# Kernel optimization log

Hardware: AMD Instinct MI355X
Metric: run time of the kernel (lower is better)

## Reference

```python
import jax, jax.numpy as jnp
import numpy as np

N, K = 4096, 256          # rays, samples per ray
V = 100000                # voxel table size
D = 64                    # field MLP hidden dim
SCALER = 7.0              # free-energy scaler from the source


def setup_inputs() -> dict:
    key = jax.random.key(0)
    ks = jax.random.split(key, 12)
    ray_start = jax.random.normal(ks[0], (N, 3), jnp.float32)
    rd = jax.random.normal(ks[1], (N, 3), jnp.float32)
    ray_dir = rd / jnp.linalg.norm(rd, axis=-1, keepdims=True)
    sampled_depth = jnp.sort(
        0.5 + 4.0 * jax.random.uniform(ks[2], (N, K), jnp.float32), axis=-1)
    sampled_dists = 0.02 * jax.random.uniform(ks[3], (N, K), jnp.float32)
    raw = jax.random.randint(ks[4], (N, K), 0, V + V // 4)
    sampled_idx = jnp.where(raw < V, raw, -1).astype(jnp.int64)
    voxel_color = 0.1 * jax.random.normal(ks[5], (V, 3), jnp.float32)
    W1 = jax.random.normal(ks[6], (6, D), jnp.float32) * (1.0 / np.sqrt(6.0))
    b1 = jnp.zeros((D,), jnp.float32)
    w_sigma = jax.random.normal(ks[7], (D, 1), jnp.float32) * (1.0 / np.sqrt(D))
    b_sigma = jnp.zeros((1,), jnp.float32)
    W_tex = jax.random.normal(ks[8], (D, 3), jnp.float32) * (1.0 / np.sqrt(D))
    b_tex = jnp.zeros((3,), jnp.float32)
    return dict(ray_start=ray_start, ray_dir=ray_dir,
                sampled_depth=sampled_depth, sampled_dists=sampled_dists,
                sampled_idx=sampled_idx, voxel_color=voxel_color,
                W1=W1, b1=b1, w_sigma=w_sigma, b_sigma=b_sigma,
                W_tex=W_tex, b_tex=b_tex)


def reference(ray_start, ray_dir, sampled_depth, sampled_dists, sampled_idx,
              voxel_color, W1, b1, w_sigma, b_sigma, W_tex, b_tex):
    mask = sampled_idx != -1                                   # [N,K] sample_mask
    # sampled_xyz = ray(start, dir, depth); sampled_dir broadcast of ray_dir
    xyz = ray_start[:, None, :] + ray_dir[:, None, :] * sampled_depth[..., None]
    dirs = jnp.broadcast_to(ray_dir[:, None, :], xyz.shape)    # [N,K,3]
    feat = jnp.concatenate([xyz, dirs], axis=-1)               # [N,K,6]
    # field_fn: small MLP -> sigma, texture
    h = jax.nn.relu(jnp.einsum('nkf,fd->nkd', feat, W1) + b1)  # [N,K,D]
    sigma = (jnp.einsum('nkd,do->nko', h, w_sigma) + b_sigma)[..., 0]  # [N,K]
    # voxel color embedding lookup (F.embedding); res=True adds it to texture
    idx_safe = jnp.where(mask, sampled_idx, 0)
    vcol = voxel_color[idx_safe]                               # [N,K,3] gather
    texture = jnp.einsum('nkd,dc->nkc', h, W_tex) + b_tex + vcol
    # free energy; masked_scatter == zero-out where mask is False
    free_energy = jnp.where(mask,
                            jax.nn.relu(sigma) * sampled_dists * SCALER, 0.0)
    texture = jnp.where(mask[..., None], texture, 0.0)
    # alpha compositing: a = 1-exp(-fe), b = exp(-cumsum(shifted fe))
    shifted = jnp.concatenate(
        [jnp.zeros((free_energy.shape[0], 1), free_energy.dtype),
         free_energy[:, :-1]], axis=-1)
    a = 1.0 - jnp.exp(-free_energy)
    b = jnp.exp(-jnp.cumsum(shifted, axis=-1))
    probs = a * b                                              # [N,K]
    depths = jnp.sum(sampled_depth * probs, axis=-1)           # [N]
    missed = 1.0 - jnp.sum(probs, axis=-1)                     # [N]
    colors = jnp.sum(texture * probs[..., None], axis=-2)      # [N,3]
    return colors, depths, missed, probs
```

## Files before the change

kernel.cpp:

```cpp
#include <hip/hip_runtime.h>

#define K_SAMP 256
#define D_HID 64
#define SCALER_FE 7.0f

typedef _Float16 half8  __attribute__((ext_vector_type(8)));
typedef __fp16   fp16x2 __attribute__((ext_vector_type(2)));
typedef float    f32x4  __attribute__((ext_vector_type(4)));

union H8U { half8 h; uint u[4]; };
union H8P { fp16x2 h2[4]; half8 h8; };

__device__ __forceinline__ half8 h8zero() {
    half8 a;
    #pragma unroll
    for (int j = 0; j < 8; ++j) a[j] = (_Float16)0.f;
    return a;
}

#define DPP_ADD(x, ctrl, rowmask)                                              \
    (x) += __int_as_float(__builtin_amdgcn_update_dpp(                         \
        0, __float_as_int(x), (ctrl), (rowmask), 0xf, false))

__device__ __forceinline__ float dpp_scan_incl(float x) {
    DPP_ADD(x, 0x111, 0xf);
    DPP_ADD(x, 0x112, 0xf);
    DPP_ADD(x, 0x114, 0xf);
    DPP_ADD(x, 0x118, 0xf);
    DPP_ADD(x, 0x142, 0xa);
    DPP_ADD(x, 0x143, 0xc);
    return x;
}

__global__ __launch_bounds__(256, 4)
void volrend_kernel(const float* __restrict__ ray_start,
                    const float* __restrict__ ray_dir,
                    const float* __restrict__ depth,
                    const float* __restrict__ dists,
                    const int*   __restrict__ vidx,
                    const float* __restrict__ vcol_tab,
                    const float* __restrict__ W1,
                    const float* __restrict__ b1,
                    const float* __restrict__ w_sigma,
                    const float* __restrict__ b_sigma,
                    const float* __restrict__ W_tex,
                    const float* __restrict__ b_tex,
                    float* __restrict__ out_colors,
                    float* __restrict__ out_depths,
                    float* __restrict__ out_missed,
                    float* __restrict__ out_probs) {
    __shared__ uint  sFragP[4][6 * 64];
    __shared__ float sOutP[4][4 * K_SAMP];

    const int tid  = threadIdx.x;
    const int lane = tid & 63;
    const int wv   = tid >> 6;
    const int ray  = __builtin_amdgcn_readfirstlane(blockIdx.x * 4 + wv);
    const int m    = lane & 15;
    const int g    = lane >> 4;

    if (tid < 64) {
        #pragma unroll
        for (int tt = 0; tt < 4; ++tt) {
            const int dim = 8 * (m >> 2) + (m & 3) + 4 * (tt & 1) + 32 * (tt >> 1);
            half8 a = h8zero();
            if (g == 0) {
                #pragma unroll
                for (int j = 0; j < 6; ++j) a[j] = (_Float16)W1[j * D_HID + dim];
                a[6] = (_Float16)b1[dim];
            }
            H8U c; c.h = a;
            #pragma unroll
            for (int k = 0; k < 4; ++k) sFragP[k][tt * 64 + lane] = c.u[k];
        }
        half8 a2a = h8zero(), a2b = h8zero();
        if (m < 4) {
            const int c = (m >= 1) ? (m - 1) : 0;
            #pragma unroll
            for (int j = 0; j < 8; ++j) {
                const int d = 8 * g + j;
                a2a[j] = (_Float16)((m == 0) ? w_sigma[d]      : W_tex[d * 3 + c]);
                a2b[j] = (_Float16)((m == 0) ? w_sigma[d + 32] : W_tex[(d + 32) * 3 + c]);
            }
        }
        H8U ca; ca.h = a2a;
        H8U cb; cb.h = a2b;
        #pragma unroll
        for (int k = 0; k < 4; ++k) {
            sFragP[k][4 * 64 + lane] = ca.u[k];
            sFragP[k][5 * 64 + lane] = cb.u[k];
        }
    }

    const float rs0 = ray_start[ray * 3 + 0];
    const float rs1 = ray_start[ray * 3 + 1];
    const float rs2 = ray_start[ray * 3 + 2];
    const float rd0 = ray_dir[ray * 3 + 0];
    const float rd1 = ray_dir[ray * 3 + 1];
    const float rd2 = ray_dir[ray * 3 + 2];
    const float bs  = b_sigma[0];
    const float bt0 = b_tex[0], bt1 = b_tex[1], bt2 = b_tex[2];

    const size_t rayBase = (size_t)ray * K_SAMP;
    float dep_[4], dst_[4];
    int   vi_[4];
    #pragma unroll
    for (int s = 0; s < 4; ++s) {
        const int n = lane + 64 * s;
        dep_[s] = depth[rayBase + n];
        dst_[s] = dists[rayBase + n];
        vi_[s]  = vidx[rayBase + n];
    }
    bool  msk[4];
    float vc[4][3];
    #pragma unroll
    for (int s = 0; s < 4; ++s) {
        msk[s] = (vi_[s] != -1);
        const int b = (msk[s] ? vi_[s] : 0) * 3;
        vc[s][0] = vcol_tab[b + 0];
        vc[s][1] = vcol_tab[b + 1];
        vc[s][2] = vcol_tab[b + 2];
    }

    __syncthreads();

    half8 a1[4];
    #pragma unroll
    for (int tt = 0; tt < 4; ++tt) {
        H8U c;
        #pragma unroll
        for (int k = 0; k < 4; ++k) c.u[k] = sFragP[k][tt * 64 + lane];
        a1[tt] = c.h;
    }
    H8U ca, cb;
    #pragma unroll
    for (int k = 0; k < 4; ++k) {
        ca.u[k] = sFragP[k][4 * 64 + lane];
        cb.u[k] = sFragP[k][5 * 64 + lane];
    }
    const half8 a2a = ca.h;
    const half8 a2b = cb.h;

    f32x4 oinit = {0.f, 0.f, 0.f, 0.f};
    if (g == 0) { oinit[0] = bs; oinit[1] = bt0; oinit[2] = bt1; oinit[3] = bt2; }
    const f32x4 zero4 = {0.f, 0.f, 0.f, 0.f};

    const fp16x2 hc12 = __builtin_amdgcn_cvt_pkrtz(rd1, rd2);
    const fp16x2 hc3  = __builtin_amdgcn_cvt_pkrtz(1.0f, 0.0f);

    #pragma unroll 4
    for (int t = 0; t < 16; ++t) {
        const float dpt = depth[rayBase + 16 * t + m];
        const float fx = fmaf(rd0, dpt, rs0);
        const float fy = fmaf(rd1, dpt, rs1);
        const float fz = fmaf(rd2, dpt, rs2);
        H8P bb;
        bb.h2[0] = __builtin_amdgcn_cvt_pkrtz(fx, fy);
        bb.h2[1] = __builtin_amdgcn_cvt_pkrtz(fz, rd0);
        bb.h2[2] = hc12;
        bb.h2[3] = hc3;
        const f32x4 h0 = __builtin_amdgcn_mfma_f32_16x16x32_f16(a1[0], bb.h8, zero4, 0, 0, 0);
        const f32x4 h1 = __builtin_amdgcn_mfma_f32_16x16x32_f16(a1[1], bb.h8, zero4, 0, 0, 0);
        const f32x4 h2 = __builtin_amdgcn_mfma_f32_16x16x32_f16(a1[2], bb.h8, zero4, 0, 0, 0);
        const f32x4 h3 = __builtin_amdgcn_mfma_f32_16x16x32_f16(a1[3], bb.h8, zero4, 0, 0, 0);

        H8P p2a, p2b;
        p2a.h2[0] = __builtin_amdgcn_cvt_pkrtz(fmaxf(h0[0], 0.f), fmaxf(h0[1], 0.f));
        p2a.h2[1] = __builtin_amdgcn_cvt_pkrtz(fmaxf(h0[2], 0.f), fmaxf(h0[3], 0.f));
        p2a.h2[2] = __builtin_amdgcn_cvt_pkrtz(fmaxf(h1[0], 0.f), fmaxf(h1[1], 0.f));
        p2a.h2[3] = __builtin_amdgcn_cvt_pkrtz(fmaxf(h1[2], 0.f), fmaxf(h1[3], 0.f));
        p2b.h2[0] = __builtin_amdgcn_cvt_pkrtz(fmaxf(h2[0], 0.f), fmaxf(h2[1], 0.f));
        p2b.h2[1] = __builtin_amdgcn_cvt_pkrtz(fmaxf(h2[2], 0.f), fmaxf(h2[3], 0.f));
        p2b.h2[2] = __builtin_amdgcn_cvt_pkrtz(fmaxf(h3[0], 0.f), fmaxf(h3[1], 0.f));
        p2b.h2[3] = __builtin_amdgcn_cvt_pkrtz(fmaxf(h3[2], 0.f), fmaxf(h3[3], 0.f));

        f32x4 o = oinit;
        o = __builtin_amdgcn_mfma_f32_16x16x32_f16(a2a, p2a.h8, o, 0, 0, 0);
        o = __builtin_amdgcn_mfma_f32_16x16x32_f16(a2b, p2b.h8, o, 0, 0, 0);

        if (g == 0) {
            const int idx = (wv << 8) + 16 * t + m;
            sOutP[0][idx] = o[0];
            sOutP[1][idx] = o[1];
            sOutP[2][idx] = o[2];
            sOutP[3][idx] = o[3];
        }
    }

    float fe_[4], tA[4], tB[4], tC[4];
    #pragma unroll
    for (int s = 0; s < 4; ++s) {
        const int idx = (wv << 8) + lane + 64 * s;
        const float sg = sOutP[0][idx];
        const float u0 = sOutP[1][idx];
        const float u1 = sOutP[2][idx];
        const float u2 = sOutP[3][idx];
        if (msk[s]) {
            fe_[s] = fmaxf(sg, 0.f) * dst_[s] * SCALER_FE;
            tA[s] = u0 + vc[s][0];
            tB[s] = u1 + vc[s][1];
            tC[s] = u2 + vc[s][2];
        } else {
            fe_[s] = 0.f; tA[s] = 0.f; tB[s] = 0.f; tC[s] = 0.f;
        }
    }

    float incl[4], tot[4];
    #pragma unroll
    for (int s = 0; s < 4; ++s) incl[s] = dpp_scan_incl(fe_[s]);
    #pragma unroll
    for (int s = 0; s < 4; ++s) tot[s] = __shfl(incl[s], 63, 64);

    float p_[4];
    float base = 0.f;
    #pragma unroll
    for (int s = 0; s < 4; ++s) {
        const float e = base + incl[s] - fe_[s];
        p_[s] = (1.0f - __expf(-fe_[s])) * __expf(-e);
        base += tot[s];
    }
    #pragma unroll
    for (int s = 0; s < 4; ++s) {
        out_probs[rayBase + lane + 64 * s] = p_[s];
    }

    float sp = dpp_scan_incl(p_[0] + p_[1] + p_[2] + p_[3]);
    float sd = dpp_scan_incl(dep_[0] * p_[0] + dep_[1] * p_[1] +
                             dep_[2] * p_[2] + dep_[3] * p_[3]);
    float c0 = dpp_scan_incl(tA[0] * p_[0] + tA[1] * p_[1] + tA[2] * p_[2] + tA[3] * p_[3]);
    float c1 = dpp_scan_incl(tB[0] * p_[0] + tB[1] * p_[1] + tB[2] * p_[2] + tB[3] * p_[3]);
    float c2 = dpp_scan_incl(tC[0] * p_[0] + tC[1] * p_[1] + tC[2] * p_[2] + tC[3] * p_[3]);
    if (lane == 63) {
        out_colors[ray * 3 + 0] = c0;
        out_colors[ray * 3 + 1] = c1;
        out_colors[ray * 3 + 2] = c2;
        out_depths[ray] = sd;
        out_missed[ray] = 1.0f - sp;
    }
}

extern "C" void kernel_launch(void* const* d_in, const int* in_sizes, int n_in,
                              void* d_out, int out_size, void* d_ws, size_t ws_size,
                              hipStream_t stream) {
    const float* ray_start  = (const float*)d_in[0];
    const float* ray_dir    = (const float*)d_in[1];
    const float* depth      = (const float*)d_in[2];
    const float* dists      = (const float*)d_in[3];
    const int*   vidx       = (const int*)d_in[4];
    const float* vcol       = (const float*)d_in[5];
    const float* W1         = (const float*)d_in[6];
    const float* b1         = (const float*)d_in[7];
    const float* w_sigma    = (const float*)d_in[8];
    const float* b_sigma    = (const float*)d_in[9];
    const float* W_tex      = (const float*)d_in[10];
    const float* b_tex      = (const float*)d_in[11];

    const int N = in_sizes[0] / 3;
    float* out        = (float*)d_out;
    float* out_colors = out;
    float* out_depths = out + (size_t)N * 3;
    float* out_missed = out + (size_t)N * 3 + N;
    float* out_probs  = out + (size_t)N * 3 + 2 * (size_t)N;

    volrend_kernel<<<N / 4, 256, 0, stream>>>(
        ray_start, ray_dir, depth, dists, vidx, vcol,
        W1, b1, w_sigma, b_sigma, W_tex, b_tex,
        out_colors, out_depths, out_missed, out_probs);
}
```

Baseline: 19.88 us.

## Split fused kernel into per-ray MLP kernel and compositing kernel via workspace

The single fused kernel is split in two. The first is an MLP kernel that launches one block per ray, with four waves each handling 64 samples, and writes per-sample free energy and texture as float4 to a global workspace. The second is a compositing kernel that reads the workspace back and performs the scan and reductions. This aims to raise parallelism and occupancy in the MLP phase, which was serialised over 16 tiles per wave. In exchange it adds a 16 MB workspace round-trip through memory and a second kernel launch.

```diff
diff --git a/kernel.cpp b/kernel.cpp
--- a/kernel.cpp
+++ b/kernel.cpp
@@ -32,30 +32,26 @@
     return x;
 }
 
-__global__ __launch_bounds__(256, 4)
-void volrend_kernel(const float* __restrict__ ray_start,
-                    const float* __restrict__ ray_dir,
-                    const float* __restrict__ depth,
-                    const float* __restrict__ dists,
-                    const int*   __restrict__ vidx,
-                    const float* __restrict__ vcol_tab,
-                    const float* __restrict__ W1,
-                    const float* __restrict__ b1,
-                    const float* __restrict__ w_sigma,
-                    const float* __restrict__ b_sigma,
-                    const float* __restrict__ W_tex,
-                    const float* __restrict__ b_tex,
-                    float* __restrict__ out_colors,
-                    float* __restrict__ out_depths,
-                    float* __restrict__ out_missed,
-                    float* __restrict__ out_probs) {
-    __shared__ uint  sFragP[4][6 * 64];
-    __shared__ float sOutP[4][4 * K_SAMP];
+__global__ __launch_bounds__(256, 6)
+void volrend_mlp(const float* __restrict__ ray_start,
+                 const float* __restrict__ ray_dir,
+                 const float* __restrict__ depth,
+                 const float* __restrict__ dists,
+                 const int*   __restrict__ vidx,
+                 const float* __restrict__ vcol_tab,
+                 const float* __restrict__ W1,
+                 const float* __restrict__ b1,
+                 const float* __restrict__ w_sigma,
+                 const float* __restrict__ b_sigma,
+                 const float* __restrict__ W_tex,
+                 const float* __restrict__ b_tex,
+                 float4* __restrict__ ws) {
+    __shared__ uint sFragP[4][6 * 64];
 
     const int tid  = threadIdx.x;
     const int lane = tid & 63;
     const int wv   = tid >> 6;
-    const int ray  = __builtin_amdgcn_readfirstlane(blockIdx.x * 4 + wv);
+    const int ray  = blockIdx.x;
     const int m    = lane & 15;
     const int g    = lane >> 4;
 
@@ -101,27 +97,6 @@
     const float bs  = b_sigma[0];
     const float bt0 = b_tex[0], bt1 = b_tex[1], bt2 = b_tex[2];
 
-    const size_t rayBase = (size_t)ray * K_SAMP;
-    float dep_[4], dst_[4];
-    int   vi_[4];
-    #pragma unroll
-    for (int s = 0; s < 4; ++s) {
-        const int n = lane + 64 * s;
-        dep_[s] = depth[rayBase + n];
-        dst_[s] = dists[rayBase + n];
-        vi_[s]  = vidx[rayBase + n];
-    }
-    bool  msk[4];
-    float vc[4][3];
-    #pragma unroll
-    for (int s = 0; s < 4; ++s) {
-        msk[s] = (vi_[s] != -1);
-        const int b = (msk[s] ? vi_[s] : 0) * 3;
-        vc[s][0] = vcol_tab[b + 0];
-        vc[s][1] = vcol_tab[b + 1];
-        vc[s][2] = vcol_tab[b + 2];
-    }
-
     __syncthreads();
 
     half8 a1[4];
@@ -148,9 +123,12 @@
     const fp16x2 hc12 = __builtin_amdgcn_cvt_pkrtz(rd1, rd2);
     const fp16x2 hc3  = __builtin_amdgcn_cvt_pkrtz(1.0f, 0.0f);
 
-    #pragma unroll 4
-    for (int t = 0; t < 16; ++t) {
-        const float dpt = depth[rayBase + 16 * t + m];
+    const size_t rayBase = (size_t)ray * K_SAMP;
+
+    #pragma unroll
+    for (int t = 0; t < 4; ++t) {
+        const int   n   = (wv << 6) + 16 * t + m;
+        const float dpt = depth[rayBase + n];
         const float fx = fmaf(rd0, dpt, rs0);
         const float fy = fmaf(rd1, dpt, rs1);
         const float fz = fmaf(rd2, dpt, rs2);
@@ -179,30 +157,41 @@
         o = __builtin_amdgcn_mfma_f32_16x16x32_f16(a2b, p2b.h8, o, 0, 0, 0);
 
         if (g == 0) {
-            const int idx = (wv << 8) + 16 * t + m;
-            sOutP[0][idx] = o[0];
-            sOutP[1][idx] = o[1];
-            sOutP[2][idx] = o[2];
-            sOutP[3][idx] = o[3];
-        }
-    }
-
-    float fe_[4], tA[4], tB[4], tC[4];
+            const float dstv = dists[rayBase + n];
+            const int   viv  = vidx[rayBase + n];
+            const bool  mk   = (viv != -1);
+            const int   vb   = (mk ? viv : 0) * 3;
+            float fe = 0.f, tA = 0.f, tB = 0.f, tC = 0.f;
+            if (mk) {
+                fe = fmaxf(o[0], 0.f) * dstv * SCALER_FE;
+                tA = o[1] + vcol_tab[vb + 0];
+                tB = o[2] + vcol_tab[vb + 1];
+                tC = o[3] + vcol_tab[vb + 2];
+            }
+            ws[rayBase + n] = make_float4(fe, tA, tB, tC);
+        }
+    }
+}
+
+__global__ __launch_bounds__(256, 8)
+void volrend_comp(const float4* __restrict__ ws,
+                  const float*  __restrict__ depth,
+                  float* __restrict__ out_colors,
+                  float* __restrict__ out_depths,
+                  float* __restrict__ out_missed,
+                  float* __restrict__ out_probs) {
+    const int lane = threadIdx.x & 63;
+    const int wv   = threadIdx.x >> 6;
+    const int ray  = __builtin_amdgcn_readfirstlane(blockIdx.x * 4 + wv);
+    const size_t rayBase = (size_t)ray * K_SAMP;
+
+    float fe_[4], tA[4], tB[4], tC[4], dep_[4];
     #pragma unroll
     for (int s = 0; s < 4; ++s) {
-        const int idx = (wv << 8) + lane + 64 * s;
-        const float sg = sOutP[0][idx];
-        const float u0 = sOutP[1][idx];
-        const float u1 = sOutP[2][idx];
-        const float u2 = sOutP[3][idx];
-        if (msk[s]) {
-            fe_[s] = fmaxf(sg, 0.f) * dst_[s] * SCALER_FE;
-            tA[s] = u0 + vc[s][0];
-            tB[s] = u1 + vc[s][1];
-            tC[s] = u2 + vc[s][2];
-        } else {
-            fe_[s] = 0.f; tA[s] = 0.f; tB[s] = 0.f; tC[s] = 0.f;
-        }
+        const int n = lane + 64 * s;
+        const float4 f4 = ws[rayBase + n];
+        dep_[s] = depth[rayBase + n];
+        fe_[s] = f4.x; tA[s] = f4.y; tB[s] = f4.z; tC[s] = f4.w;
     }
 
     float incl[4], tot[4];
@@ -261,9 +250,11 @@
     float* out_depths = out + (size_t)N * 3;
     float* out_missed = out + (size_t)N * 3 + N;
     float* out_probs  = out + (size_t)N * 3 + 2 * (size_t)N;
-
-    volrend_kernel<<<N / 4, 256, 0, stream>>>(
+    float4* ws = (float4*)d_ws;
+
+    volrend_mlp<<<N, 256, 0, stream>>>(
         ray_start, ray_dir, depth, dists, vidx, vcol,
-        W1, b1, w_sigma, b_sigma, W_tex, b_tex,
-        out_colors, out_depths, out_missed, out_probs);
-}
+        W1, b1, w_sigma, b_sigma, W_tex, b_tex, ws);
+    volrend_comp<<<N / 4, 256, 0, stream>>>(
+        ws, depth, out_colors, out_depths, out_missed, out_probs);
+}
```

Result: slower. 29.03 us (+46.0%).

## Switch MLP matmuls from 16x16x32 to 32x32x16 MFMA tiles

Applied to the files above, without the earlier changes.

Replaces the 16x16x32 f16 MFMA layout with 32x32x16 MFMAs that process 32 samples per step. The first layer now takes 2 MFMAs per 32 samples instead of 4 per 16, and the second layer takes 4 chained MFMAs per 32 samples instead of 2 per 16. Weight fragments are rebuilt for the new operand layout, and the upper half-wave gets zero B inputs because K only covers 8 features. The instruction count per sample drops slightly, but the larger MFMAs have longer latency, need 16-wide accumulators that raise register pressure, and waste half the K dimension on zeros.

```diff
diff --git a/kernel.cpp b/kernel.cpp
--- a/kernel.cpp
+++ b/kernel.cpp
@@ -6,7 +6,7 @@
 
 typedef _Float16 half8  __attribute__((ext_vector_type(8)));
 typedef __fp16   fp16x2 __attribute__((ext_vector_type(2)));
-typedef float    f32x4  __attribute__((ext_vector_type(4)));
+typedef float    f32x16 __attribute__((ext_vector_type(16)));
 
 union H8U { half8 h; uint u[4]; };
 union H8P { fp16x2 h2[4]; half8 h8; };
@@ -56,39 +56,38 @@
     const int lane = tid & 63;
     const int wv   = tid >> 6;
     const int ray  = __builtin_amdgcn_readfirstlane(blockIdx.x * 4 + wv);
-    const int m    = lane & 15;
-    const int g    = lane >> 4;
+    const int col  = lane & 31;
+    const int g2   = lane >> 5;
 
     if (tid < 64) {
-        #pragma unroll
-        for (int tt = 0; tt < 4; ++tt) {
-            const int dim = 8 * (m >> 2) + (m & 3) + 4 * (tt & 1) + 32 * (tt >> 1);
+        const int x = lane & 31;
+        #pragma unroll
+        for (int T = 0; T < 2; ++T) {
             half8 a = h8zero();
-            if (g == 0) {
+            if (lane < 32) {
+                const int dim = 16 * (x >> 3) + 8 * ((x >> 2) & 1) + 4 * T + (x & 3);
                 #pragma unroll
                 for (int j = 0; j < 6; ++j) a[j] = (_Float16)W1[j * D_HID + dim];
                 a[6] = (_Float16)b1[dim];
             }
             H8U c; c.h = a;
             #pragma unroll
-            for (int k = 0; k < 4; ++k) sFragP[k][tt * 64 + lane] = c.u[k];
-        }
-        half8 a2a = h8zero(), a2b = h8zero();
-        if (m < 4) {
-            const int c = (m >= 1) ? (m - 1) : 0;
+            for (int k = 0; k < 4; ++k) sFragP[k][T * 64 + lane] = c.u[k];
+        }
+        #pragma unroll
+        for (int q = 0; q < 4; ++q) {
+            half8 a = h8zero();
+            if (x < 4) {
+                const int dbase = 16 * q + 8 * (lane >> 5);
+                #pragma unroll
+                for (int j = 0; j < 8; ++j) {
+                    const int d = dbase + j;
+                    a[j] = (_Float16)((x == 0) ? w_sigma[d] : W_tex[d * 3 + (x - 1)]);
+                }
+            }
+            H8U c; c.h = a;
             #pragma unroll
-            for (int j = 0; j < 8; ++j) {
-                const int d = 8 * g + j;
-                a2a[j] = (_Float16)((m == 0) ? w_sigma[d]      : W_tex[d * 3 + c]);
-                a2b[j] = (_Float16)((m == 0) ? w_sigma[d + 32] : W_tex[(d + 32) * 3 + c]);
-            }
-        }
-        H8U ca; ca.h = a2a;
-        H8U cb; cb.h = a2b;
-        #pragma unroll
-        for (int k = 0; k < 4; ++k) {
-            sFragP[k][4 * 64 + lane] = ca.u[k];
-            sFragP[k][5 * 64 + lane] = cb.u[k];
+            for (int k = 0; k < 4; ++k) sFragP[k][(2 + q) * 64 + lane] = c.u[k];
         }
     }
 
@@ -124,62 +123,66 @@
 
     __syncthreads();
 
-    half8 a1[4];
-    #pragma unroll
-    for (int tt = 0; tt < 4; ++tt) {
+    half8 a1[2], a2[4];
+    #pragma unroll
+    for (int T = 0; T < 2; ++T) {
         H8U c;
         #pragma unroll
-        for (int k = 0; k < 4; ++k) c.u[k] = sFragP[k][tt * 64 + lane];
-        a1[tt] = c.h;
-    }
-    H8U ca, cb;
-    #pragma unroll
-    for (int k = 0; k < 4; ++k) {
-        ca.u[k] = sFragP[k][4 * 64 + lane];
-        cb.u[k] = sFragP[k][5 * 64 + lane];
-    }
-    const half8 a2a = ca.h;
-    const half8 a2b = cb.h;
-
-    f32x4 oinit = {0.f, 0.f, 0.f, 0.f};
-    if (g == 0) { oinit[0] = bs; oinit[1] = bt0; oinit[2] = bt1; oinit[3] = bt2; }
-    const f32x4 zero4 = {0.f, 0.f, 0.f, 0.f};
+        for (int k = 0; k < 4; ++k) c.u[k] = sFragP[k][T * 64 + lane];
+        a1[T] = c.h;
+    }
+    #pragma unroll
+    for (int q = 0; q < 4; ++q) {
+        H8U c;
+        #pragma unroll
+        for (int k = 0; k < 4; ++k) c.u[k] = sFragP[k][(2 + q) * 64 + lane];
+        a2[q] = c.h;
+    }
+
+    f32x16 zero16;
+    #pragma unroll
+    for (int k = 0; k < 16; ++k) zero16[k] = 0.f;
+    f32x16 oinit = zero16;
+    if (lane < 32) { oinit[0] = bs; oinit[1] = bt0; oinit[2] = bt1; oinit[3] = bt2; }
 
     const fp16x2 hc12 = __builtin_amdgcn_cvt_pkrtz(rd1, rd2);
     const fp16x2 hc3  = __builtin_amdgcn_cvt_pkrtz(1.0f, 0.0f);
-
-    #pragma unroll 4
-    for (int t = 0; t < 16; ++t) {
-        const float dpt = depth[rayBase + 16 * t + m];
+    const half8  bnull = h8zero();
+
+    #pragma unroll 2
+    for (int t = 0; t < 8; ++t) {
+        const int   n   = 32 * t + col;
+        const float dpt = depth[rayBase + n];
         const float fx = fmaf(rd0, dpt, rs0);
         const float fy = fmaf(rd1, dpt, rs1);
         const float fz = fmaf(rd2, dpt, rs2);
-        H8P bb;
-        bb.h2[0] = __builtin_amdgcn_cvt_pkrtz(fx, fy);
-        bb.h2[1] = __builtin_amdgcn_cvt_pkrtz(fz, rd0);
-        bb.h2[2] = hc12;
-        bb.h2[3] = hc3;
-        const f32x4 h0 = __builtin_amdgcn_mfma_f32_16x16x32_f16(a1[0], bb.h8, zero4, 0, 0, 0);
-        const f32x4 h1 = __builtin_amdgcn_mfma_f32_16x16x32_f16(a1[1], bb.h8, zero4, 0, 0, 0);
-        const f32x4 h2 = __builtin_amdgcn_mfma_f32_16x16x32_f16(a1[2], bb.h8, zero4, 0, 0, 0);
-        const f32x4 h3 = __builtin_amdgcn_mfma_f32_16x16x32_f16(a1[3], bb.h8, zero4, 0, 0, 0);
-
-        H8P p2a, p2b;
-        p2a.h2[0] = __builtin_amdgcn_cvt_pkrtz(fmaxf(h0[0], 0.f), fmaxf(h0[1], 0.f));
-        p2a.h2[1] = __builtin_amdgcn_cvt_pkrtz(fmaxf(h0[2], 0.f), fmaxf(h0[3], 0.f));
-        p2a.h2[2] = __builtin_amdgcn_cvt_pkrtz(fmaxf(h1[0], 0.f), fmaxf(h1[1], 0.f));
-        p2a.h2[3] = __builtin_amdgcn_cvt_pkrtz(fmaxf(h1[2], 0.f), fmaxf(h1[3], 0.f));
-        p2b.h2[0] = __builtin_amdgcn_cvt_pkrtz(fmaxf(h2[0], 0.f), fmaxf(h2[1], 0.f));
-        p2b.h2[1] = __builtin_amdgcn_cvt_pkrtz(fmaxf(h2[2], 0.f), fmaxf(h2[3], 0.f));
-        p2b.h2[2] = __builtin_amdgcn_cvt_pkrtz(fmaxf(h3[0], 0.f), fmaxf(h3[1], 0.f));
-        p2b.h2[3] = __builtin_amdgcn_cvt_pkrtz(fmaxf(h3[2], 0.f), fmaxf(h3[3], 0.f));
-
-        f32x4 o = oinit;
-        o = __builtin_amdgcn_mfma_f32_16x16x32_f16(a2a, p2a.h8, o, 0, 0, 0);
-        o = __builtin_amdgcn_mfma_f32_16x16x32_f16(a2b, p2b.h8, o, 0, 0, 0);
-
-        if (g == 0) {
-            const int idx = (wv << 8) + 16 * t + m;
+        H8P bbu;
+        bbu.h2[0] = __builtin_amdgcn_cvt_pkrtz(fx, fy);
+        bbu.h2[1] = __builtin_amdgcn_cvt_pkrtz(fz, rd0);
+        bbu.h2[2] = hc12;
+        bbu.h2[3] = hc3;
+        const half8 bb = (lane < 32) ? bbu.h8 : bnull;
+
+        const f32x16 c1a = __builtin_amdgcn_mfma_f32_32x32x16_f16(a1[0], bb, zero16, 0, 0, 0);
+        const f32x16 c1b = __builtin_amdgcn_mfma_f32_32x32x16_f16(a1[1], bb, zero16, 0, 0, 0);
+
+        f32x16 o = oinit;
+        #pragma unroll
+        for (int q = 0; q < 4; ++q) {
+            H8P b2;
+            b2.h2[0] = __builtin_amdgcn_cvt_pkrtz(fmaxf(c1a[4 * q + 0], 0.f),
+                                                  fmaxf(c1a[4 * q + 1], 0.f));
+            b2.h2[1] = __builtin_amdgcn_cvt_pkrtz(fmaxf(c1a[4 * q + 2], 0.f),
+                                                  fmaxf(c1a[4 * q + 3], 0.f));
+            b2.h2[2] = __builtin_amdgcn_cvt_pkrtz(fmaxf(c1b[4 * q + 0], 0.f),
+                                                  fmaxf(c1b[4 * q + 1], 0.f));
+            b2.h2[3] = __builtin_amdgcn_cvt_pkrtz(fmaxf(c1b[4 * q + 2], 0.f),
+                                                  fmaxf(c1b[4 * q + 3], 0.f));
+            o = __builtin_amdgcn_mfma_f32_32x32x16_f16(a2[q], b2.h8, o, 0, 0, 0);
+        }
+
+        if (lane < 32) {
+            const int idx = (wv << 8) + n;
             sOutP[0][idx] = o[0];
             sOutP[1][idx] = o[1];
             sOutP[2][idx] = o[2];
```

After: 18.97 us. 1.05x faster.
